# Kernel tuning notes

Hardware: AMD Instinct MI355X
Metric: run time of the kernel (lower is better)

The kernel has to match this reference:

```python
import math
import jax, jax.numpy as jnp
import numpy as np
from jax import lax

SQRT2 = math.sqrt(2.0)


def _conv2d(x, w, stride=1, padding=0):
    # x: [N,C,H,W], w: [O,I,kh,kw]
    return lax.conv_general_dilated(
        x, w,
        window_strides=(stride, stride),
        padding=[(padding, padding), (padding, padding)],
        dimension_numbers=('NCHW', 'OIHW', 'NCHW'))


def _fused_leaky_relu(x, bias, slope=0.2):
    # add per-channel bias, leaky relu, scale by sqrt(2) (StyleGAN2 FusedLeakyReLU)
    y = x + bias.reshape(1, -1, 1, 1)
    return jnp.where(y >= 0, y, slope * y) * SQRT2


def _upsample2x_bilinear(x):
    # matches torch F.interpolate(scale_factor=2, mode='bilinear', align_corners=False)
    n, c, h, w = x.shape
    return jax.image.resize(x, (n, c, 2 * h, 2 * w), method='bilinear')


def setup_inputs() -> dict:
    key = jax.random.key(0)
    k = jax.random.split(key, 5)
    Cin, Cout = 256, 128
    x = jax.random.normal(k[0], (8, Cin, 64, 64), dtype=jnp.float32)
    w1 = jax.random.normal(k[1], (Cin, Cin, 3, 3), dtype=jnp.float32)
    b1 = jnp.zeros((Cin,), dtype=jnp.float32)
    w2 = jax.random.normal(k[2], (Cout, Cin, 3, 3), dtype=jnp.float32)
    b2 = jnp.zeros((Cout,), dtype=jnp.float32)
    w_skip = jax.random.normal(k[3], (Cout, Cin, 1, 1), dtype=jnp.float32)
    return {"x": x, "w1": w1, "b1": b1, "w2": w2, "b2": b2, "w_skip": w_skip}


def reference(x, w1, b1, w2, b2, w_skip):
    Cin = x.shape[1]
    scale3 = 1.0 / math.sqrt(Cin * 9)  # equalized lr scale for 3x3
    scale1 = 1.0 / math.sqrt(Cin * 1)  # for 1x1 skip

    # conv1: EqualConv2d(in,in,3,pad=1,bias=False) + FusedLeakyReLU
    out = _conv2d(x, w1 * scale3, stride=1, padding=1)
    out = _fused_leaky_relu(out, b1)

    # conv2: bilinear up x2 + EqualConv(in,out,3,pad=1,no bias) + FusedLeakyReLU
    out = _upsample2x_bilinear(out)
    out = _conv2d(out, w2 * scale3, stride=1, padding=1)
    out = _fused_leaky_relu(out, b2)

    # skip: bilinear up x2 + 1x1 equalized conv, no bias/activation
    skip = _upsample2x_bilinear(x)
    skip = _conv2d(skip, w_skip * scale1, stride=1, padding=0)

    return (out + skip) / SQRT2
```

## Files before the change

kernel.cpp:

```cpp
#include <hip/hip_runtime.h>
#include <hip/hip_bf16.h>


typedef __attribute__((ext_vector_type(8))) short bf16x8;
typedef __attribute__((ext_vector_type(4))) float f32x4;

#define SQRT2F  1.41421356237309504880f
#define RSQRT2F 0.70710678118654752440f

__device__ __forceinline__ float lrelu_s(float v) { return v >= 0.f ? v : 0.2f * v; }

__device__ __forceinline__ unsigned short f2bf(float f) {
    unsigned u = __builtin_bit_cast(unsigned, f);
    u += 0x7fffu + ((u >> 16) & 1u);
    return (unsigned short)(u >> 16);
}
__device__ __forceinline__ float bflo(unsigned u) {
    return __builtin_bit_cast(float, u << 16);
}
__device__ __forceinline__ float bfhi(unsigned u) {
    return __builtin_bit_cast(float, u & 0xffff0000u);
}

__device__ __forceinline__ void up2_coef(int o, int lim, int& i0, int& i1, float& w0, float& w1) {
    int h = o >> 1;
    if (o & 1) { i0 = h; i1 = (h + 1 > lim) ? lim : h + 1; w0 = 0.75f; w1 = 0.25f; }
    else       { i0 = (h - 1 < 0) ? 0 : h - 1; i1 = h;     w0 = 0.25f; w1 = 0.75f; }
}

__global__ __launch_bounds__(256) void k_wt3(const float* __restrict__ w,
                                             unsigned short* __restrict__ wt,
                                             int total, float scale) {
    int i = blockIdx.x * 256 + threadIdx.x;
    if (i >= total) return;
    int cp  = i & 7;
    int t1i = i >> 3;  int ocp = t1i & 63;
    int t2i = t1i >> 6; int q  = t2i & 3;
    int t3  = t2i >> 2; int tap = t3 % 9;
    int t4  = t3 / 9;   int ci  = t4 & 7; int ocb = t4 >> 3;
    int oc = (ocb << 6) + ocp;
    int c  = (ci << 5) + (q << 3) + cp;
    wt[i] = f2bf(w[(oc * 256 + c) * 9 + tap] * scale);
}

__global__ __launch_bounds__(256) void k_wt1(const float* __restrict__ w,
                                             unsigned short* __restrict__ wt,
                                             int total, float scale) {
    int i = blockIdx.x * 256 + threadIdx.x;
    if (i >= total) return;
    wt[i] = f2bf(w[i] * scale);
}

__global__ __launch_bounds__(256) void k_xprep(const float* __restrict__ x,
                                               unsigned short* __restrict__ xT) {
    __shared__ float t[64][65];
    const int n = blockIdx.z, c0 = blockIdx.y << 6, p0 = blockIdx.x << 6;
    for (int i = threadIdx.x; i < 4096; i += 256) {
        int c = i >> 6, p = i & 63;
        t[c][p] = x[((size_t)(n * 256 + c0 + c) << 12) + p0 + p];
    }
    __syncthreads();
    for (int i = threadIdx.x; i < 4096; i += 256) {
        int p = i >> 6, c = i & 63;
        xT[((size_t)((n << 12) + p0 + p) << 8) + c0 + c] = f2bf(t[c][p]);
    }
}

__global__ __launch_bounds__(256, 2) void k_conv1(
    const unsigned short* __restrict__ xT, const unsigned short* __restrict__ w1T,
    const float* __restrict__ b1, unsigned short* __restrict__ t1)
{
    __shared__ __align__(16) unsigned short dt[6][66][40];
    __shared__ __align__(16) unsigned short wl[18432];
    const int tid = threadIdx.x;
    const int n   = blockIdx.x >> 4;
    const int y0  = (blockIdx.x & 15) << 2;
    const int ocb = blockIdx.y;
    const int oc0 = ocb << 6;
    const int w   = tid >> 6;
    const int m   = tid & 15;
    const int q   = (tid & 63) >> 4;

    f32x4 acc[4][4];
#pragma unroll
    for (int a = 0; a < 4; ++a)
#pragma unroll
        for (int g = 0; g < 4; ++g) acc[a][g] = (f32x4){0.f, 0.f, 0.f, 0.f};

    const unsigned short* wsrc = w1T + (size_t)ocb * 147456;
    const unsigned short* xTn  = xT + ((size_t)n << 20);
    unsigned short* dtf = &dt[0][0][0];

    int goff[7], ldsoff[7];
#pragma unroll
    for (int k = 0; k < 7; ++k) {
        int idx = tid + (k << 8);
        goff[k] = -1; ldsoff[k] = -1;
        if (idx < 1584) {
            int r = idx / 264; int rem = idx - r * 264; int col = rem >> 2; int g = rem & 3;
            ldsoff[k] = (r * 66 + col) * 40 + (g << 3);
            int gy = y0 - 1 + r, gx = col - 1;
            if ((unsigned)gy < 64u && (unsigned)gx < 64u)
                goff[k] = (((gy << 6) + gx) << 8) + (g << 3);
        }
    }

    uint4 vreg[7];
#pragma unroll
    for (int k = 0; k < 7; ++k) {
        vreg[k] = make_uint4(0, 0, 0, 0);
        if (goff[k] >= 0) vreg[k] = *(const uint4*)(xTn + goff[k]);
    }

    for (int ci = 0; ci < 8; ++ci) {
        uint4 twreg[9];
        const unsigned short* wc = wsrc + ci * 18432;
#pragma unroll
        for (int j = 0; j < 9; ++j)
            twreg[j] = *(const uint4*)(wc + ((tid + (j << 8)) << 3));
#pragma unroll
        for (int k = 0; k < 7; ++k)
            if (ldsoff[k] >= 0) *(uint4*)(dtf + ldsoff[k]) = vreg[k];
        if (ci < 7) {
            const int cn = (ci + 1) << 5;
#pragma unroll
            for (int k = 0; k < 7; ++k)
                if (goff[k] >= 0) vreg[k] = *(const uint4*)(xTn + goff[k] + cn);
        }
#pragma unroll
        for (int j = 0; j < 9; ++j)
            *(uint4*)(wl + ((tid + (j << 8)) << 3)) = twreg[j];
        __syncthreads();

#pragma unroll
        for (int tap = 0; tap < 9; ++tap) {
            const int dy = tap / 3, dx = tap - 3 * (tap / 3);
            bf16x8 bfr[4];
#pragma unroll
            for (int g = 0; g < 4; ++g)
                bfr[g] = *(const bf16x8*)(&dt[w + dy][(g << 4) + m + dx][q << 3]);
#pragma unroll
            for (int a = 0; a < 4; ++a) {
                bf16x8 af = *(const bf16x8*)(wl + (((((tap << 2) + q) << 6) + (a << 4) + m) << 3));
#pragma unroll
                for (int g = 0; g < 4; ++g)
                    acc[a][g] = __builtin_amdgcn_mfma_f32_16x16x32_bf16(af, bfr[g], acc[a][g], 0, 0, 0);
            }
        }
        __syncthreads();
    }

    const int y = y0 + w;
#pragma unroll
    for (int a = 0; a < 4; ++a) {
        const int oc = oc0 + (a << 4) + (q << 2);
        float b0 = b1[oc], b1v = b1[oc + 1], b2v = b1[oc + 2], b3 = b1[oc + 3];
#pragma unroll
        for (int g = 0; g < 4; ++g) {
            const int xcol = (g << 4) + m;
            unsigned lo = (unsigned)f2bf(lrelu_s(acc[a][g][0] + b0) * SQRT2F)
                        | ((unsigned)f2bf(lrelu_s(acc[a][g][1] + b1v) * SQRT2F) << 16);
            unsigned hi = (unsigned)f2bf(lrelu_s(acc[a][g][2] + b2v) * SQRT2F)
                        | ((unsigned)f2bf(lrelu_s(acc[a][g][3] + b3) * SQRT2F) << 16);
            uint2 s; s.x = lo; s.y = hi;
            *(uint2*)(t1 + (((n << 12) + (y << 6) + xcol) << 8) + oc) = s;
        }
    }
}

__global__ __launch_bounds__(256, 2) void k_skip(
    const unsigned short* __restrict__ xT, const unsigned short* __restrict__ wsT,
    unsigned short* __restrict__ t2)
{
    const int tid = threadIdx.x;
    const int w = tid >> 6, m = tid & 15, q = (tid & 63) >> 4;
    const int px0 = blockIdx.x << 6;
    const int apx = px0 + (w << 4) + m;

    f32x4 acc[8];
#pragma unroll
    for (int g = 0; g < 8; ++g) acc[g] = (f32x4){0.f, 0.f, 0.f, 0.f};

#pragma unroll
    for (int c0 = 0; c0 < 256; c0 += 32) {
        bf16x8 af = *(const bf16x8*)(xT + ((size_t)apx << 8) + c0 + (q << 3));
#pragma unroll
        for (int g = 0; g < 8; ++g) {
            bf16x8 bf = *(const bf16x8*)(wsT + (((g << 4) + m) << 8) + c0 + (q << 3));
            acc[g] = __builtin_amdgcn_mfma_f32_16x16x32_bf16(af, bf, acc[g], 0, 0, 0);
        }
    }
#pragma unroll
    for (int g = 0; g < 8; ++g) {
        const int oc = (g << 4) + m;
#pragma unroll
        for (int r = 0; r < 4; ++r) {
            int opx = px0 + (w << 4) + (q << 2) + r;
            t2[((size_t)opx << 7) + oc] = f2bf(acc[g][r]);
        }
    }
}

__global__ __launch_bounds__(256) void k_synthu(
    const unsigned short* __restrict__ t1, unsigned short* __restrict__ u)
{
    const int n = blockIdx.z, oy = blockIdx.y, x0 = blockIdx.x << 6;
    int ry0, ry1; float wy0, wy1;
    up2_coef(oy, 63, ry0, ry1, wy0, wy1);
    const unsigned short* tb = t1 + ((size_t)n << 20);
    unsigned short* ub = u + ((size_t)((n << 7) + oy) << 15);

    for (int idx = threadIdx.x; idx < 2048; idx += 256) {
        const int ox = x0 + (idx >> 5), g = idx & 31;
        int cx0, cx1; float wx0, wx1;
        up2_coef(ox, 63, cx0, cx1, wx0, wx1);
        const int co = g << 3;
        uint4 v00 = *(const uint4*)(tb + (((ry0 << 6) + cx0) << 8) + co);
        uint4 v01 = *(const uint4*)(tb + (((ry0 << 6) + cx1) << 8) + co);
        uint4 v10 = *(const uint4*)(tb + (((ry1 << 6) + cx0) << 8) + co);
        uint4 v11 = *(const uint4*)(tb + (((ry1 << 6) + cx1) << 8) + co);
        const unsigned* pa = (const unsigned*)&v00; const unsigned* pb = (const unsigned*)&v01;
        const unsigned* pc = (const unsigned*)&v10; const unsigned* pd = (const unsigned*)&v11;
        uint4 res; unsigned* pr = (unsigned*)&res;
#pragma unroll
        for (int j = 0; j < 4; ++j) {
            float vlo = wy0 * (wx0 * bflo(pa[j]) + wx1 * bflo(pb[j]))
                      + wy1 * (wx0 * bflo(pc[j]) + wx1 * bflo(pd[j]));
            float vhi = wy0 * (wx0 * bfhi(pa[j]) + wx1 * bfhi(pb[j]))
                      + wy1 * (wx0 * bfhi(pc[j]) + wx1 * bfhi(pd[j]));
            pr[j] = (unsigned)f2bf(vlo) | ((unsigned)f2bf(vhi) << 16);
        }
        *(uint4*)(ub + (ox << 8) + co) = res;
    }
}

__global__ __launch_bounds__(256, 2) void k_conv2u(
    const unsigned short* __restrict__ u, const unsigned short* __restrict__ w2T,
    const unsigned short* __restrict__ t2, const float* __restrict__ b2,
    float* __restrict__ out)
{
    __shared__ __align__(16) unsigned short dt[6][66][40];
    __shared__ __align__(16) unsigned short wl[18432];
    const int tid  = threadIdx.x;
    const int n    = blockIdx.x >> 6;
    const int rest = blockIdx.x & 63;
    const int oy0  = (rest >> 1) << 2;
    const int x0   = (rest & 1) << 6;
    const int ocb  = blockIdx.y;
    const int oc0  = ocb << 6;
    const int w    = tid >> 6;
    const int m    = tid & 15;
    const int q    = (tid & 63) >> 4;

    f32x4 acc[4][4];
#pragma unroll
    for (int a = 0; a < 4; ++a)
#pragma unroll
        for (int g = 0; g < 4; ++g) acc[a][g] = (f32x4){0.f, 0.f, 0.f, 0.f};

    const unsigned short* wsrc = w2T + (size_t)ocb * 147456;
    const unsigned short* ub   = u + ((size_t)n << 22);
    unsigned short* dtf = &dt[0][0][0];

    int goff[7], ldsoff[7];
#pragma unroll
    for (int k = 0; k < 7; ++k) {
        int idx = tid + (k << 8);
        goff[k] = -1; ldsoff[k] = -1;
        if (idx < 1584) {
            int r = idx / 264; int rem = idx - r * 264; int col = rem >> 2; int g = rem & 3;
            ldsoff[k] = (r * 66 + col) * 40 + (g << 3);
            int gy = oy0 - 1 + r, gx = x0 - 1 + col;
            if ((unsigned)gy < 128u && (unsigned)gx < 128u)
                goff[k] = (((gy << 7) + gx) << 8) + (g << 3);
        }
    }

    uint4 vreg[7];
#pragma unroll
    for (int k = 0; k < 7; ++k) {
        vreg[k] = make_uint4(0, 0, 0, 0);
        if (goff[k] >= 0) vreg[k] = *(const uint4*)(ub + goff[k]);
    }

    for (int ci = 0; ci < 8; ++ci) {
        uint4 twreg[9];
        const unsigned short* wc = wsrc + ci * 18432;
#pragma unroll
        for (int j = 0; j < 9; ++j)
            twreg[j] = *(const uint4*)(wc + ((tid + (j << 8)) << 3));
#pragma unroll
        for (int k = 0; k < 7; ++k)
            if (ldsoff[k] >= 0) *(uint4*)(dtf + ldsoff[k]) = vreg[k];
        if (ci < 7) {
            const int cn = (ci + 1) << 5;
#pragma unroll
            for (int k = 0; k < 7; ++k)
                if (goff[k] >= 0) vreg[k] = *(const uint4*)(ub + goff[k] + cn);
        }
#pragma unroll
        for (int j = 0; j < 9; ++j)
            *(uint4*)(wl + ((tid + (j << 8)) << 3)) = twreg[j];
        __syncthreads();

#pragma unroll
        for (int tap = 0; tap < 9; ++tap) {
            const int dy = tap / 3, dx = tap - 3 * (tap / 3);
            bf16x8 bfr[4];
#pragma unroll
            for (int g = 0; g < 4; ++g)
                bfr[g] = *(const bf16x8*)(&dt[w + dy][(g << 4) + m + dx][q << 3]);
#pragma unroll
            for (int a = 0; a < 4; ++a) {
                bf16x8 af = *(const bf16x8*)(wl + (((((tap << 2) + q) << 6) + (a << 4) + m) << 3));
#pragma unroll
                for (int g = 0; g < 4; ++g)
                    acc[a][g] = __builtin_amdgcn_mfma_f32_16x16x32_bf16(af, bfr[g], acc[a][g], 0, 0, 0);
            }
        }
        __syncthreads();
    }

    const int oy = oy0 + w;
    int ry0, ry1; float wy0, wy1;
    up2_coef(oy, 63, ry0, ry1, wy0, wy1);
    const unsigned short* t2b = t2 + ((size_t)n << 19);
#pragma unroll
    for (int a = 0; a < 4; ++a) {
        const int oc = oc0 + (a << 4) + (q << 2);
        float bb[4] = {b2[oc], b2[oc + 1], b2[oc + 2], b2[oc + 3]};
        float* pbase = out + ((size_t)(((n << 7) + oc) << 7) + oy) * 128;
#pragma unroll
        for (int g = 0; g < 4; ++g) {
            const int ox = x0 + (g << 4) + m;
            int cx0, cx1; float wx0, wx1;
            up2_coef(ox, 63, cx0, cx1, wx0, wx1);
            uint2 A = *(const uint2*)(t2b + (((ry0 << 6) + cx0) << 7) + oc);
            uint2 B = *(const uint2*)(t2b + (((ry0 << 6) + cx1) << 7) + oc);
            uint2 C = *(const uint2*)(t2b + (((ry1 << 6) + cx0) << 7) + oc);
            uint2 D = *(const uint2*)(t2b + (((ry1 << 6) + cx1) << 7) + oc);
            const unsigned* pA = (const unsigned*)&A; const unsigned* pB = (const unsigned*)&B;
            const unsigned* pC = (const unsigned*)&C; const unsigned* pD = (const unsigned*)&D;
#pragma unroll
            for (int r = 0; r < 4; ++r) {
                unsigned wa = pA[r >> 1], wb = pB[r >> 1], wc_ = pC[r >> 1], wd = pD[r >> 1];
                float va = (r & 1) ? bfhi(wa) : bflo(wa);
                float vb = (r & 1) ? bfhi(wb) : bflo(wb);
                float vc = (r & 1) ? bfhi(wc_) : bflo(wc_);
                float vd = (r & 1) ? bfhi(wd) : bflo(wd);
                float sk = wy0 * (wx0 * va + wx1 * vb) + wy1 * (wx0 * vc + wx1 * vd);
                pbase[(size_t)r * 16384 + ox] = lrelu_s(acc[a][g][r] + bb[r]) + sk * RSQRT2F;
            }
        }
    }
}

extern "C" void kernel_launch(void* const* d_in, const int* in_sizes, int n_in,
                              void* d_out, int out_size, void* d_ws, size_t ws_size,
                              hipStream_t stream)
{
    const float* x   = (const float*)d_in[0];
    const float* w1  = (const float*)d_in[1];
    const float* b1  = (const float*)d_in[2];
    const float* w2  = (const float*)d_in[3];
    const float* b2  = (const float*)d_in[4];
    const float* wsk = (const float*)d_in[5];
    float* out = (float*)d_out;

    unsigned short* xT  = (unsigned short*)d_ws;
    unsigned short* t1  = xT + 8388608;
    unsigned short* t2  = t1 + 8388608;
    unsigned short* w1T = t2 + 4194304;
    unsigned short* w2T = w1T + 589824;
    unsigned short* wsT = w2T + 294912;
    unsigned short* u   = wsT + 32768;

    k_wt3   <<<dim3(2304), 256, 0, stream>>>(w1, w1T, 589824, 1.0f / 48.0f);
    k_wt3   <<<dim3(1152), 256, 0, stream>>>(w2, w2T, 294912, 1.0f / 48.0f);
    k_wt1   <<<dim3(128),  256, 0, stream>>>(wsk, wsT, 32768, 1.0f / 16.0f);
    k_xprep <<<dim3(64, 4, 8), 256, 0, stream>>>(x, xT);
    k_conv1 <<<dim3(128, 4), 256, 0, stream>>>(xT, w1T, b1, t1);
    k_skip  <<<dim3(512), 256, 0, stream>>>(xT, wsT, t2);
    k_synthu<<<dim3(2, 128, 8), 256, 0, stream>>>(t1, u);
    k_conv2u<<<dim3(512, 2), 256, 0, stream>>>(u, w2T, t2, b2, out);
}
```

Baseline: 283.5 us.

## Load conv weight fragments directly from global memory, dropping LDS weight staging

Both conv kernels stop staging the 36KB per-chunk weight tile in shared memory. Each lane now loads its own MFMA A-fragments straight from global/L2, double-buffered one tap ahead. Launch bounds rise from 2 to 3 blocks per CU, since LDS use per block shrinks to the activation tile. The trade is redundant weight reads across the four waves of a block (every wave loads the same fragments), plus more global load latency inside the MFMA loop, in exchange for higher occupancy and fewer LDS writes.

```diff
diff --git a/kernel.cpp b/kernel.cpp
--- a/kernel.cpp
+++ b/kernel.cpp
@@ -66,12 +66,11 @@
     }
 }
 
-__global__ __launch_bounds__(256, 2) void k_conv1(
+__global__ __launch_bounds__(256, 3) void k_conv1(
     const unsigned short* __restrict__ xT, const unsigned short* __restrict__ w1T,
     const float* __restrict__ b1, unsigned short* __restrict__ t1)
 {
     __shared__ __align__(16) unsigned short dt[6][66][40];
-    __shared__ __align__(16) unsigned short wl[18432];
     const int tid = threadIdx.x;
     const int n   = blockIdx.x >> 4;
     const int y0  = (blockIdx.x & 15) << 2;
@@ -90,6 +89,7 @@
     const unsigned short* wsrc = w1T + (size_t)ocb * 147456;
     const unsigned short* xTn  = xT + ((size_t)n << 20);
     unsigned short* dtf = &dt[0][0][0];
+    const int loff = ((q << 6) + m) << 3;
 
     int goff[7], ldsoff[7];
 #pragma unroll
@@ -113,11 +113,7 @@
     }
 
     for (int ci = 0; ci < 8; ++ci) {
-        uint4 twreg[9];
-        const unsigned short* wc = wsrc + ci * 18432;
-#pragma unroll
-        for (int j = 0; j < 9; ++j)
-            twreg[j] = *(const uint4*)(wc + ((tid + (j << 8)) << 3));
+        const unsigned short* wci = wsrc + ci * 18432;
 #pragma unroll
         for (int k = 0; k < 7; ++k)
             if (ldsoff[k] >= 0) *(uint4*)(dtf + ldsoff[k]) = vreg[k];
@@ -127,13 +123,20 @@
             for (int k = 0; k < 7; ++k)
                 if (goff[k] >= 0) vreg[k] = *(const uint4*)(xTn + goff[k] + cn);
         }
-#pragma unroll
-        for (int j = 0; j < 9; ++j)
-            *(uint4*)(wl + ((tid + (j << 8)) << 3)) = twreg[j];
+        uint4 aq[2][4];
+#pragma unroll
+        for (int a = 0; a < 4; ++a)
+            aq[0][a] = *(const uint4*)(wci + loff + (a << 7));
         __syncthreads();
 
 #pragma unroll
         for (int tap = 0; tap < 9; ++tap) {
+            const int cur = tap & 1;
+            if (tap < 8) {
+#pragma unroll
+                for (int a = 0; a < 4; ++a)
+                    aq[cur ^ 1][a] = *(const uint4*)(wci + loff + (a << 7) + ((tap + 1) << 11));
+            }
             const int dy = tap / 3, dx = tap - 3 * (tap / 3);
             bf16x8 bfr[4];
 #pragma unroll
@@ -141,7 +144,7 @@
                 bfr[g] = *(const bf16x8*)(&dt[w + dy][(g << 4) + m + dx][q << 3]);
 #pragma unroll
             for (int a = 0; a < 4; ++a) {
-                bf16x8 af = *(const bf16x8*)(wl + (((((tap << 2) + q) << 6) + (a << 4) + m) << 3));
+                bf16x8 af = __builtin_bit_cast(bf16x8, aq[cur][a]);
 #pragma unroll
                 for (int g = 0; g < 4; ++g)
                     acc[a][g] = __builtin_amdgcn_mfma_f32_16x16x32_bf16(af, bfr[g], acc[a][g], 0, 0, 0);
@@ -234,13 +237,12 @@
     }
 }
 
-__global__ __launch_bounds__(256, 2) void k_conv2u(
+__global__ __launch_bounds__(256, 3) void k_conv2u(
     const unsigned short* __restrict__ u, const unsigned short* __restrict__ w2T,
     const unsigned short* __restrict__ t2, const float* __restrict__ b2,
     float* __restrict__ out)
 {
     __shared__ __align__(16) unsigned short dt[6][66][40];
-    __shared__ __align__(16) unsigned short wl[18432];
     const int tid  = threadIdx.x;
     const int n    = blockIdx.x >> 6;
     const int rest = blockIdx.x & 63;
@@ -261,6 +263,7 @@
     const unsigned short* wsrc = w2T + (size_t)ocb * 147456;
     const unsigned short* ub   = u + ((size_t)n << 22);
     unsigned short* dtf = &dt[0][0][0];
+    const int loff = ((q << 6) + m) << 3;
 
     int goff[7], ldsoff[7];
 #pragma unroll
@@ -284,11 +287,7 @@
     }
 
     for (int ci = 0; ci < 8; ++ci) {
-        uint4 twreg[9];
-        const unsigned short* wc = wsrc + ci * 18432;
-#pragma unroll
-        for (int j = 0; j < 9; ++j)
-            twreg[j] = *(const uint4*)(wc + ((tid + (j << 8)) << 3));
+        const unsigned short* wci = wsrc + ci * 18432;
 #pragma unroll
         for (int k = 0; k < 7; ++k)
             if (ldsoff[k] >= 0) *(uint4*)(dtf + ldsoff[k]) = vreg[k];
@@ -298,13 +297,20 @@
             for (int k = 0; k < 7; ++k)
                 if (goff[k] >= 0) vreg[k] = *(const uint4*)(ub + goff[k] + cn);
         }
-#pragma unroll
-        for (int j = 0; j < 9; ++j)
-            *(uint4*)(wl + ((tid + (j << 8)) << 3)) = twreg[j];
+        uint4 aq[2][4];
+#pragma unroll
+        for (int a = 0; a < 4; ++a)
+            aq[0][a] = *(const uint4*)(wci + loff + (a << 7));
         __syncthreads();
 
 #pragma unroll
         for (int tap = 0; tap < 9; ++tap) {
+            const int cur = tap & 1;
+            if (tap < 8) {
+#pragma unroll
+                for (int a = 0; a < 4; ++a)
+                    aq[cur ^ 1][a] = *(const uint4*)(wci + loff + (a << 7) + ((tap + 1) << 11));
+            }
             const int dy = tap / 3, dx = tap - 3 * (tap / 3);
             bf16x8 bfr[4];
 #pragma unroll
@@ -312,7 +318,7 @@
                 bfr[g] = *(const bf16x8*)(&dt[w + dy][(g << 4) + m + dx][q << 3]);
 #pragma unroll
             for (int a = 0; a < 4; ++a) {
-                bf16x8 af = *(const bf16x8*)(wl + (((((tap << 2) + q) << 6) + (a << 4) + m) << 3));
+                bf16x8 af = __builtin_bit_cast(bf16x8, aq[cur][a]);
 #pragma unroll
                 for (int g = 0; g < 4; ++g)
                     acc[a][g] = __builtin_amdgcn_mfma_f32_16x16x32_bf16(af, bfr[g], acc[a][g], 0, 0, 0);
```

Result: slower. 412.9 us (+45.6%).
